# Kernel tuning notes

Hardware: AMD Instinct MI355X
Metric: run time of the kernel (lower is better)

Reference implementation:

```python
import jax, jax.numpy as jnp
import numpy as np

TOKENS, DIM, N_EXPERTS, TOPK = 8192, 4096, 256, 8

def setup_inputs() -> dict:
    key = jax.random.key(0)
    k1, k2 = jax.random.split(key)
    x = jax.random.normal(k1, (TOKENS, DIM), dtype=jnp.float32)
    weight = jax.random.normal(k2, (N_EXPERTS, DIM), dtype=jnp.float32) * (DIM ** -0.5)
    return {"x": x, "weight": weight}

def reference(x, weight):
    # logits: [tokens, n_experts]
    logits = jnp.einsum('td,ed->te', x, weight)
    scores = jax.nn.sigmoid(logits)
    topv, indices = jax.lax.top_k(scores, TOPK)          # [tokens, topk]
    gates = topv / jnp.sum(topv, axis=-1, keepdims=True)
    return gates, indices
```

## Files before the change

### kernel.cpp

```cpp
#include <hip/hip_runtime.h>
#include <hip/hip_bf16.h>
#include <hip/hip_fp16.h>
#include <math.h>

#define TOKENS   8192
#define DIM      4096
#define NEXP     256
#define TOPK     8
#define CAND     12

#define MT4      64
#define BK3      64
#define KG       (DIM / 32)

typedef _Float16 f16x8 __attribute__((ext_vector_type(8)));
typedef float    f32x4 __attribute__((ext_vector_type(4)));

typedef const __attribute__((address_space(1))) unsigned int* gas_ptr;
typedef       __attribute__((address_space(3))) unsigned int* las_ptr;

__global__ __launch_bounds__(256)
void convert_w(const float* __restrict__ w, _Float16* __restrict__ whs) {
    const int g = blockIdx.x * 256 + threadIdx.x;
    const int tile = g >> 6, c = g & 63;
    const int q = c >> 4, r = c & 15;
    const int ng = tile / KG, kg = tile % KG;
    const int n = ng * 16 + r, k = kg * 32 + q * 8;
    const float4 a = *(const float4*)(w + (size_t)n * DIM + k);
    const float4 b = *(const float4*)(w + (size_t)n * DIM + k + 4);
    f16x8 h;
    h[0] = (_Float16)a.x; h[1] = (_Float16)a.y;
    h[2] = (_Float16)a.z; h[3] = (_Float16)a.w;
    h[4] = (_Float16)b.x; h[5] = (_Float16)b.y;
    h[6] = (_Float16)b.z; h[7] = (_Float16)b.w;
    *(f16x8*)(whs + (size_t)g * 8) = h;
}

__global__ __launch_bounds__(256, 3)
void gemm_v4(const float* __restrict__ x, const _Float16* __restrict__ whs,
             float* __restrict__ logits, int kspan) {
    __shared__ _Float16 As[8 * 512];
    __shared__ _Float16 Bs[32 * 512];

    const int t = threadIdx.x, w = t >> 6, lane = t & 63;
    const int m0 = blockIdx.x * MT4;
    const int kb = blockIdx.y * kspan;
    float* lp    = logits + (size_t)blockIdx.y * TOKENS * NEXP;

    const int am  = t >> 2;
    const int ack = (t & 3) * 2;
    const int amg = am >> 4, amr = am & 15;
    const int aoff0 = ((amg * 2 + (ack >> 2)) * 64 + (ack & 3) * 16 + amr) * 8;
    const int ack1  = ack + 1;
    const int aoff1 = ((amg * 2 + (ack1 >> 2)) * 64 + (ack1 & 3) * 16 + amr) * 8;

    f32x4 acc[4][4];
    #pragma unroll
    for (int i = 0; i < 4; ++i)
        #pragma unroll
        for (int j = 0; j < 4; ++j) acc[i][j] = (f32x4){0.f, 0.f, 0.f, 0.f};

    const float* xrow = x + (size_t)(m0 + am) * DIM + ack * 8;
    float4 xr0 = *(const float4*)(xrow + kb);
    float4 xr1 = *(const float4*)(xrow + kb + 4);
    float4 xr2 = *(const float4*)(xrow + kb + 8);
    float4 xr3 = *(const float4*)(xrow + kb + 12);

    for (int k0 = kb; k0 < kb + kspan; k0 += BK3) {
        #pragma unroll
        for (int c = 0; c < 8; ++c) {
            const int ti  = w * 8 + c;
            const int ng  = ti >> 1, kgl = ti & 1;
            const _Float16* gp = whs + ((size_t)(ng * KG + (k0 >> 5) + kgl)) * 512
                                     + lane * 8;
            __builtin_amdgcn_global_load_lds((gas_ptr)gp, (las_ptr)&Bs[ti * 512],
                                             16, 0, 0);
        }
        {
            f16x8 h0, h1;
            h0[0] = (_Float16)xr0.x; h0[1] = (_Float16)xr0.y;
            h0[2] = (_Float16)xr0.z; h0[3] = (_Float16)xr0.w;
            h0[4] = (_Float16)xr1.x; h0[5] = (_Float16)xr1.y;
            h0[6] = (_Float16)xr1.z; h0[7] = (_Float16)xr1.w;
            h1[0] = (_Float16)xr2.x; h1[1] = (_Float16)xr2.y;
            h1[2] = (_Float16)xr2.z; h1[3] = (_Float16)xr2.w;
            h1[4] = (_Float16)xr3.x; h1[5] = (_Float16)xr3.y;
            h1[6] = (_Float16)xr3.z; h1[7] = (_Float16)xr3.w;
            *(f16x8*)&As[aoff0] = h0;
            *(f16x8*)&As[aoff1] = h1;
        }
        __syncthreads();

        if (k0 + BK3 < kb + kspan) {
            xr0 = *(const float4*)(xrow + k0 + BK3);
            xr1 = *(const float4*)(xrow + k0 + BK3 + 4);
            xr2 = *(const float4*)(xrow + k0 + BK3 + 8);
            xr3 = *(const float4*)(xrow + k0 + BK3 + 12);
        }

        #pragma unroll
        for (int kk = 0; kk < 2; ++kk) {
            f16x8 af[4], bf[4];
            #pragma unroll
            for (int mt = 0; mt < 4; ++mt)
                af[mt] = *(const f16x8*)&As[((mt * 2 + kk) * 64 + lane) * 8];
            #pragma unroll
            for (int nt = 0; nt < 4; ++nt)
                bf[nt] = *(const f16x8*)&Bs[(((w * 4 + nt) * 2 + kk) * 64 + lane) * 8];
            #pragma unroll
            for (int mt = 0; mt < 4; ++mt)
                #pragma unroll
                for (int nt = 0; nt < 4; ++nt)
                    acc[mt][nt] = __builtin_amdgcn_mfma_f32_16x16x32_f16(
                        af[mt], bf[nt], acc[mt][nt], 0, 0, 0);
        }
        __syncthreads();
    }

    #pragma unroll
    for (int mt = 0; mt < 4; ++mt) {
        #pragma unroll
        for (int nt = 0; nt < 4; ++nt) {
            #pragma unroll
            for (int r = 0; r < 4; ++r) {
                const int m = m0 + mt * 16 + (lane >> 4) * 4 + r;
                const int n = (w * 4 + nt) * 16 + (lane & 15);
                lp[(size_t)m * NEXP + n] = acc[mt][nt][r];
            }
        }
    }
}

__global__ __launch_bounds__(256)
void topk_cand(const float* __restrict__ logits, int* __restrict__ cand,
               int nsplit) {
    const int lane  = threadIdx.x & 63;
    const int token = blockIdx.x * 4 + (threadIdx.x >> 6);
    const float* lp = logits + (size_t)token * NEXP;

    float s[4];
    #pragma unroll
    for (int j = 0; j < 4; ++j) s[j] = 0.f;
    for (int p = 0; p < nsplit; ++p) {
        const float* pp = lp + (size_t)p * TOKENS * NEXP;
        #pragma unroll
        for (int j = 0; j < 4; ++j) s[j] += pp[j * 64 + lane];
    }

    int mye = 0;
    #pragma unroll
    for (int r = 0; r < CAND; ++r) {
        float bv = s[0];
        int   be = lane;
        #pragma unroll
        for (int j = 1; j < 4; ++j) {
            if (s[j] > bv) { bv = s[j]; be = j * 64 + lane; }
        }
        #pragma unroll
        for (int off = 32; off > 0; off >>= 1) {
            const float ov = __shfl_xor(bv, off, 64);
            const int   oe = __shfl_xor(be, off, 64);
            if (ov > bv || (ov == bv && oe < be)) { bv = ov; be = oe; }
        }
        if (lane == r) mye = be;
        if ((be & 63) == lane) s[be >> 6] = -1e30f;
    }

    if (lane < CAND) cand[token * CAND + lane] = mye;
}

__global__ __launch_bounds__(256)
void rescore(const float* __restrict__ x, const float* __restrict__ w,
             const int* __restrict__ cand, float* __restrict__ out) {
    __shared__ float  xs[DIM];
    __shared__ double stot[CAND];
    __shared__ int    sce[CAND];

    const int t = threadIdx.x, wave = t >> 6, lane = t & 63;
    const int token = blockIdx.x;

    const float* xrow = x + (size_t)token * DIM;
    #pragma unroll
    for (int r = 0; r < 4; ++r) {
        const float* gp = xrow + r * 1024 + wave * 256 + lane * 4;
        __builtin_amdgcn_global_load_lds((gas_ptr)gp,
                                         (las_ptr)&xs[r * 1024 + wave * 256],
                                         16, 0, 2 );
    }

    int ce[3];
    const f32x4* wp[3];
    #pragma unroll
    for (int j = 0; j < 3; ++j) {
        ce[j] = __builtin_amdgcn_readfirstlane(cand[token * CAND + wave * 3 + j]);
        wp[j] = (const f32x4*)(w + (size_t)ce[j] * DIM);
    }

    double acc[3];
    #pragma unroll
    for (int j = 0; j < 3; ++j) acc[j] = 0.0;

    f32x4 wb[3][3];
    #pragma unroll
    for (int j = 0; j < 3; ++j) wb[0][j] = wp[j][lane];
    #pragma unroll
    for (int j = 0; j < 3; ++j) wb[1][j] = wp[j][64 + lane];

    __syncthreads();

    #pragma unroll
    for (int i = 0; i < 16; ++i) {
        const int cur = i % 3, nxt = (i + 2) % 3;
        if (i < 14) {
            const int o = lane + (i + 2) * 64;
            #pragma unroll
            for (int j = 0; j < 3; ++j) wb[nxt][j] = wp[j][o];
        }
        const f32x4 xv = *(const f32x4*)&xs[(lane + i * 64) * 4];
        const double dx = (double)xv.x, dy = (double)xv.y;
        const double dz = (double)xv.z, dw = (double)xv.w;
        #pragma unroll
        for (int j = 0; j < 3; ++j) {
            const f32x4 wv = wb[cur][j];
            acc[j] = fma(dw, (double)wv.w,
                     fma(dz, (double)wv.z,
                     fma(dy, (double)wv.y,
                     fma(dx, (double)wv.x, acc[j]))));
        }
    }

    #pragma unroll
    for (int off = 32; off > 0; off >>= 1) {
        #pragma unroll
        for (int j = 0; j < 3; ++j)
            acc[j] += __shfl_xor(acc[j], off, 64);
    }

    if (lane == 0) {
        #pragma unroll
        for (int j = 0; j < 3; ++j) {
            stot[wave * 3 + j] = acc[j];
            sce[wave * 3 + j]  = ce[j];
        }
    }
    __syncthreads();

    if (wave == 0) {
        double tt[CAND];
        int    ee[CAND];
        #pragma unroll
        for (int c = 0; c < CAND; ++c) { tt[c] = stot[c]; ee[c] = sce[c]; }

        int rank[CAND];
        #pragma unroll
        for (int c = 0; c < CAND; ++c) {
            int r = 0;
            #pragma unroll
            for (int j = 0; j < CAND; ++j) {
                if (j == c) continue;
                if (tt[j] > tt[c] || (tt[j] == tt[c] && ee[j] < ee[c])) ++r;
            }
            rank[c] = r;
        }

        float sig[CAND];
        float sum = 0.f;
        #pragma unroll
        for (int c = 0; c < CAND; ++c) {
            sig[c] = 1.0f / (1.0f + expf(-(float)tt[c]));
            if (rank[c] < TOPK) sum += sig[c];
        }

        if (lane < TOPK) {
            float g = 0.f; int ei = 0;
            #pragma unroll
            for (int c = 0; c < CAND; ++c)
                if (rank[c] == lane) { g = sig[c]; ei = ee[c]; }
            out[(size_t)token * TOPK + lane] = g / sum;
            out[(size_t)TOKENS * TOPK + (size_t)token * TOPK + lane] = (float)ei;
        }
    }
}

extern "C" void kernel_launch(void* const* d_in, const int* in_sizes, int n_in,
                              void* d_out, int out_size, void* d_ws, size_t ws_size,
                              hipStream_t stream) {
    const float* x = (const float*)d_in[0];
    const float* w = (const float*)d_in[1];
    float* out     = (float*)d_out;

    const size_t plane = (size_t)TOKENS * NEXP * sizeof(float);
    const size_t fixed = (size_t)TOKENS * CAND * sizeof(int)
                       + (size_t)NEXP * DIM * sizeof(_Float16);
    int S = 4;
    if (ws_size < 4 * plane + fixed) S = (ws_size >= 2 * plane + fixed) ? 2 : 1;

    float*     logits = (float*)d_ws;
    int*       candp  = (int*)((char*)d_ws + (size_t)S * plane);
    _Float16*  whs    = (_Float16*)((char*)candp + (size_t)TOKENS * CAND * sizeof(int));

    convert_w<<<512, 256, 0, stream>>>(w, whs);
    dim3 ggrid(TOKENS / MT4, S);
    gemm_v4<<<ggrid, 256, 0, stream>>>(x, whs, logits, DIM / S);
    topk_cand<<<TOKENS / 4, 256, 0, stream>>>(logits, candp, S);
    rescore<<<TOKENS, 256, 0, stream>>>(x, w, candp, out);
}
```

Baseline: 315.3 us.

## Fuse candidate top-k into rescore and shrink GEMM M-tile to 32 rows

Removes the separate topk_cand kernel. Each wave in rescore now sums the split-K logit planes and runs the candidate selection itself, so the candidate index buffer and one launch go away. The GEMM M-tile drops from 64 to 32 rows with a higher occupancy bound, and the rescore weight prefetch goes from 2 to 3 stages deep. The trade-offs: all four waves repeat the same top-12 selection per token, and the smaller GEMM tile reuses each loaded B tile for fewer rows, which doubles B traffic.

```diff
diff --git a/kernel.cpp b/kernel.cpp
--- a/kernel.cpp
+++ b/kernel.cpp
@@ -9,7 +9,7 @@
 #define TOPK     8
 #define CAND     12
 
-#define MT4      64
+#define MT4      32
 #define BK3      64
 #define KG       (DIM / 32)
 
@@ -36,10 +36,10 @@
     *(f16x8*)(whs + (size_t)g * 8) = h;
 }
 
-__global__ __launch_bounds__(256, 3)
+__global__ __launch_bounds__(256, 4)
 void gemm_v4(const float* __restrict__ x, const _Float16* __restrict__ whs,
              float* __restrict__ logits, int kspan) {
-    __shared__ _Float16 As[8 * 512];
+    __shared__ _Float16 As[4 * 512];
     __shared__ _Float16 Bs[32 * 512];
 
     const int t = threadIdx.x, w = t >> 6, lane = t & 63;
@@ -47,24 +47,20 @@
     const int kb = blockIdx.y * kspan;
     float* lp    = logits + (size_t)blockIdx.y * TOKENS * NEXP;
 
-    const int am  = t >> 2;
-    const int ack = (t & 3) * 2;
+    const int am  = t >> 3;
+    const int ack = t & 7;
     const int amg = am >> 4, amr = am & 15;
-    const int aoff0 = ((amg * 2 + (ack >> 2)) * 64 + (ack & 3) * 16 + amr) * 8;
-    const int ack1  = ack + 1;
-    const int aoff1 = ((amg * 2 + (ack1 >> 2)) * 64 + (ack1 & 3) * 16 + amr) * 8;
-
-    f32x4 acc[4][4];
-    #pragma unroll
-    for (int i = 0; i < 4; ++i)
+    const int aoff = ((amg * 2 + (ack >> 2)) * 64 + (ack & 3) * 16 + amr) * 8;
+
+    f32x4 acc[2][4];
+    #pragma unroll
+    for (int i = 0; i < 2; ++i)
         #pragma unroll
         for (int j = 0; j < 4; ++j) acc[i][j] = (f32x4){0.f, 0.f, 0.f, 0.f};
 
     const float* xrow = x + (size_t)(m0 + am) * DIM + ack * 8;
     float4 xr0 = *(const float4*)(xrow + kb);
     float4 xr1 = *(const float4*)(xrow + kb + 4);
-    float4 xr2 = *(const float4*)(xrow + kb + 8);
-    float4 xr3 = *(const float4*)(xrow + kb + 12);
 
     for (int k0 = kb; k0 < kb + kspan; k0 += BK3) {
         #pragma unroll
@@ -77,38 +73,31 @@
                                              16, 0, 0);
         }
         {
-            f16x8 h0, h1;
+            f16x8 h0;
             h0[0] = (_Float16)xr0.x; h0[1] = (_Float16)xr0.y;
             h0[2] = (_Float16)xr0.z; h0[3] = (_Float16)xr0.w;
             h0[4] = (_Float16)xr1.x; h0[5] = (_Float16)xr1.y;
             h0[6] = (_Float16)xr1.z; h0[7] = (_Float16)xr1.w;
-            h1[0] = (_Float16)xr2.x; h1[1] = (_Float16)xr2.y;
-            h1[2] = (_Float16)xr2.z; h1[3] = (_Float16)xr2.w;
-            h1[4] = (_Float16)xr3.x; h1[5] = (_Float16)xr3.y;
-            h1[6] = (_Float16)xr3.z; h1[7] = (_Float16)xr3.w;
-            *(f16x8*)&As[aoff0] = h0;
-            *(f16x8*)&As[aoff1] = h1;
+            *(f16x8*)&As[aoff] = h0;
         }
         __syncthreads();
 
         if (k0 + BK3 < kb + kspan) {
             xr0 = *(const float4*)(xrow + k0 + BK3);
             xr1 = *(const float4*)(xrow + k0 + BK3 + 4);
-            xr2 = *(const float4*)(xrow + k0 + BK3 + 8);
-            xr3 = *(const float4*)(xrow + k0 + BK3 + 12);
         }
 
         #pragma unroll
         for (int kk = 0; kk < 2; ++kk) {
-            f16x8 af[4], bf[4];
-            #pragma unroll
-            for (int mt = 0; mt < 4; ++mt)
+            f16x8 af[2], bf[4];
+            #pragma unroll
+            for (int mt = 0; mt < 2; ++mt)
                 af[mt] = *(const f16x8*)&As[((mt * 2 + kk) * 64 + lane) * 8];
             #pragma unroll
             for (int nt = 0; nt < 4; ++nt)
                 bf[nt] = *(const f16x8*)&Bs[(((w * 4 + nt) * 2 + kk) * 64 + lane) * 8];
             #pragma unroll
-            for (int mt = 0; mt < 4; ++mt)
+            for (int mt = 0; mt < 2; ++mt)
                 #pragma unroll
                 for (int nt = 0; nt < 4; ++nt)
                     acc[mt][nt] = __builtin_amdgcn_mfma_f32_16x16x32_f16(
@@ -118,7 +107,7 @@
     }
 
     #pragma unroll
-    for (int mt = 0; mt < 4; ++mt) {
+    for (int mt = 0; mt < 2; ++mt) {
         #pragma unroll
         for (int nt = 0; nt < 4; ++nt) {
             #pragma unroll
@@ -132,46 +121,9 @@
 }
 
 __global__ __launch_bounds__(256)
-void topk_cand(const float* __restrict__ logits, int* __restrict__ cand,
-               int nsplit) {
-    const int lane  = threadIdx.x & 63;
-    const int token = blockIdx.x * 4 + (threadIdx.x >> 6);
-    const float* lp = logits + (size_t)token * NEXP;
-
-    float s[4];
-    #pragma unroll
-    for (int j = 0; j < 4; ++j) s[j] = 0.f;
-    for (int p = 0; p < nsplit; ++p) {
-        const float* pp = lp + (size_t)p * TOKENS * NEXP;
-        #pragma unroll
-        for (int j = 0; j < 4; ++j) s[j] += pp[j * 64 + lane];
-    }
-
-    int mye = 0;
-    #pragma unroll
-    for (int r = 0; r < CAND; ++r) {
-        float bv = s[0];
-        int   be = lane;
-        #pragma unroll
-        for (int j = 1; j < 4; ++j) {
-            if (s[j] > bv) { bv = s[j]; be = j * 64 + lane; }
-        }
-        #pragma unroll
-        for (int off = 32; off > 0; off >>= 1) {
-            const float ov = __shfl_xor(bv, off, 64);
-            const int   oe = __shfl_xor(be, off, 64);
-            if (ov > bv || (ov == bv && oe < be)) { bv = ov; be = oe; }
-        }
-        if (lane == r) mye = be;
-        if ((be & 63) == lane) s[be >> 6] = -1e30f;
-    }
-
-    if (lane < CAND) cand[token * CAND + lane] = mye;
-}
-
-__global__ __launch_bounds__(256)
 void rescore(const float* __restrict__ x, const float* __restrict__ w,
-             const int* __restrict__ cand, float* __restrict__ out) {
+             const float* __restrict__ logits, float* __restrict__ out,
+             int nsplit) {
     __shared__ float  xs[DIM];
     __shared__ double stot[CAND];
     __shared__ int    sce[CAND];
@@ -189,30 +141,60 @@
     }
 
     int ce[3];
+    {
+        const float* lp = logits + (size_t)token * NEXP;
+        float s[4];
+        #pragma unroll
+        for (int j = 0; j < 4; ++j) s[j] = 0.f;
+        for (int p = 0; p < nsplit; ++p) {
+            const float* pp = lp + (size_t)p * TOKENS * NEXP;
+            #pragma unroll
+            for (int j = 0; j < 4; ++j) s[j] += pp[j * 64 + lane];
+        }
+        #pragma unroll
+        for (int r = 0; r < CAND; ++r) {
+            float bv = s[0];
+            int   be = lane;
+            #pragma unroll
+            for (int j = 1; j < 4; ++j) {
+                if (s[j] > bv) { bv = s[j]; be = j * 64 + lane; }
+            }
+            #pragma unroll
+            for (int off = 32; off > 0; off >>= 1) {
+                const float ov = __shfl_xor(bv, off, 64);
+                const int   oe = __shfl_xor(be, off, 64);
+                if (ov > bv || (ov == bv && oe < be)) { bv = ov; be = oe; }
+            }
+            if (r >= wave * 3 && r < wave * 3 + 3)
+                ce[r - wave * 3] = __builtin_amdgcn_readfirstlane(be);
+            if ((be & 63) == lane) s[be >> 6] = -1e30f;
+        }
+    }
+
     const f32x4* wp[3];
     #pragma unroll
-    for (int j = 0; j < 3; ++j) {
-        ce[j] = __builtin_amdgcn_readfirstlane(cand[token * CAND + wave * 3 + j]);
+    for (int j = 0; j < 3; ++j)
         wp[j] = (const f32x4*)(w + (size_t)ce[j] * DIM);
-    }
 
     double acc[3];
     #pragma unroll
     for (int j = 0; j < 3; ++j) acc[j] = 0.0;
 
-    f32x4 wb[3][3];
+    f32x4 wb[4][3];
     #pragma unroll
     for (int j = 0; j < 3; ++j) wb[0][j] = wp[j][lane];
     #pragma unroll
     for (int j = 0; j < 3; ++j) wb[1][j] = wp[j][64 + lane];
+    #pragma unroll
+    for (int j = 0; j < 3; ++j) wb[2][j] = wp[j][128 + lane];
 
     __syncthreads();
 
     #pragma unroll
     for (int i = 0; i < 16; ++i) {
-        const int cur = i % 3, nxt = (i + 2) % 3;
-        if (i < 14) {
-            const int o = lane + (i + 2) * 64;
+        const int cur = i & 3, nxt = (i + 3) & 3;
+        if (i < 13) {
+            const int o = lane + (i + 3) * 64;
             #pragma unroll
             for (int j = 0; j < 3; ++j) wb[nxt][j] = wp[j][o];
         }
@@ -290,18 +272,15 @@
     float* out     = (float*)d_out;
 
     const size_t plane = (size_t)TOKENS * NEXP * sizeof(float);
-    const size_t fixed = (size_t)TOKENS * CAND * sizeof(int)
-                       + (size_t)NEXP * DIM * sizeof(_Float16);
+    const size_t fixed = (size_t)NEXP * DIM * sizeof(_Float16);
     int S = 4;
     if (ws_size < 4 * plane + fixed) S = (ws_size >= 2 * plane + fixed) ? 2 : 1;
 
     float*     logits = (float*)d_ws;
-    int*       candp  = (int*)((char*)d_ws + (size_t)S * plane);
-    _Float16*  whs    = (_Float16*)((char*)candp + (size_t)TOKENS * CAND * sizeof(int));
+    _Float16*  whs    = (_Float16*)((char*)d_ws + (size_t)S * plane);
 
     convert_w<<<512, 256, 0, stream>>>(w, whs);
     dim3 ggrid(TOKENS / MT4, S);
     gemm_v4<<<ggrid, 256, 0, stream>>>(x, whs, logits, DIM / S);
-    topk_cand<<<TOKENS / 4, 256, 0, stream>>>(logits, candp, S);
-    rescore<<<TOKENS, 256, 0, stream>>>(x, w, candp, out);
-}
+    rescore<<<TOKENS, 256, 0, stream>>>(x, w, logits, out, S);
+}
```

New measurement: 337.6 us. 7.1% more time.

## Double-buffer LDS tiles in GEMM and deepen weight prefetch in rescoring

Applied to the files above, without the earlier changes.

The GEMM kernel now uses two LDS buffers for A and B. The next B tile is issued via global_load_lds and the next A tile is written while the current tile is consumed by MFMAs, which cuts one barrier per iteration. The occupancy hint drops from 3 to 2 blocks per SM to make room for the doubled shared memory. Separately, the fp64 rescoring kernel prefetches weights three iterations ahead instead of two, which raises register use in exchange for more latency hiding.

```diff
diff --git a/kernel.cpp b/kernel.cpp
--- a/kernel.cpp
+++ b/kernel.cpp
@@ -36,15 +36,16 @@
     *(f16x8*)(whs + (size_t)g * 8) = h;
 }
 
-__global__ __launch_bounds__(256, 3)
+__global__ __launch_bounds__(256, 2)
 void gemm_v4(const float* __restrict__ x, const _Float16* __restrict__ whs,
              float* __restrict__ logits, int kspan) {
-    __shared__ _Float16 As[8 * 512];
-    __shared__ _Float16 Bs[32 * 512];
+    __shared__ _Float16 As[2][8 * 512];
+    __shared__ _Float16 Bs[2][32 * 512];
 
     const int t = threadIdx.x, w = t >> 6, lane = t & 63;
     const int m0 = blockIdx.x * MT4;
     const int kb = blockIdx.y * kspan;
+    const int kend = kb + kspan;
     float* lp    = logits + (size_t)blockIdx.y * TOKENS * NEXP;
 
     const int am  = t >> 2;
@@ -61,52 +62,67 @@
         for (int j = 0; j < 4; ++j) acc[i][j] = (f32x4){0.f, 0.f, 0.f, 0.f};
 
     const float* xrow = x + (size_t)(m0 + am) * DIM + ack * 8;
-    float4 xr0 = *(const float4*)(xrow + kb);
-    float4 xr1 = *(const float4*)(xrow + kb + 4);
-    float4 xr2 = *(const float4*)(xrow + kb + 8);
-    float4 xr3 = *(const float4*)(xrow + kb + 12);
-
-    for (int k0 = kb; k0 < kb + kspan; k0 += BK3) {
+
+    auto stage_B = [&](int buf, int k0) {
         #pragma unroll
         for (int c = 0; c < 8; ++c) {
             const int ti  = w * 8 + c;
             const int ng  = ti >> 1, kgl = ti & 1;
             const _Float16* gp = whs + ((size_t)(ng * KG + (k0 >> 5) + kgl)) * 512
                                      + lane * 8;
-            __builtin_amdgcn_global_load_lds((gas_ptr)gp, (las_ptr)&Bs[ti * 512],
+            __builtin_amdgcn_global_load_lds((gas_ptr)gp,
+                                             (las_ptr)&Bs[buf][ti * 512],
                                              16, 0, 0);
         }
-        {
-            f16x8 h0, h1;
-            h0[0] = (_Float16)xr0.x; h0[1] = (_Float16)xr0.y;
-            h0[2] = (_Float16)xr0.z; h0[3] = (_Float16)xr0.w;
-            h0[4] = (_Float16)xr1.x; h0[5] = (_Float16)xr1.y;
-            h0[6] = (_Float16)xr1.z; h0[7] = (_Float16)xr1.w;
-            h1[0] = (_Float16)xr2.x; h1[1] = (_Float16)xr2.y;
-            h1[2] = (_Float16)xr2.z; h1[3] = (_Float16)xr2.w;
-            h1[4] = (_Float16)xr3.x; h1[5] = (_Float16)xr3.y;
-            h1[6] = (_Float16)xr3.z; h1[7] = (_Float16)xr3.w;
-            *(f16x8*)&As[aoff0] = h0;
-            *(f16x8*)&As[aoff1] = h1;
-        }
-        __syncthreads();
-
-        if (k0 + BK3 < kb + kspan) {
-            xr0 = *(const float4*)(xrow + k0 + BK3);
-            xr1 = *(const float4*)(xrow + k0 + BK3 + 4);
-            xr2 = *(const float4*)(xrow + k0 + BK3 + 8);
-            xr3 = *(const float4*)(xrow + k0 + BK3 + 12);
-        }
+    };
+    auto write_A = [&](int buf, const float4& r0, const float4& r1,
+                       const float4& r2, const float4& r3) {
+        f16x8 h0, h1;
+        h0[0] = (_Float16)r0.x; h0[1] = (_Float16)r0.y;
+        h0[2] = (_Float16)r0.z; h0[3] = (_Float16)r0.w;
+        h0[4] = (_Float16)r1.x; h0[5] = (_Float16)r1.y;
+        h0[6] = (_Float16)r1.z; h0[7] = (_Float16)r1.w;
+        h1[0] = (_Float16)r2.x; h1[1] = (_Float16)r2.y;
+        h1[2] = (_Float16)r2.z; h1[3] = (_Float16)r2.w;
+        h1[4] = (_Float16)r3.x; h1[5] = (_Float16)r3.y;
+        h1[6] = (_Float16)r3.z; h1[7] = (_Float16)r3.w;
+        *(f16x8*)&As[buf][aoff0] = h0;
+        *(f16x8*)&As[buf][aoff1] = h1;
+    };
+
+    {
+        float4 r0 = *(const float4*)(xrow + kb);
+        float4 r1 = *(const float4*)(xrow + kb + 4);
+        float4 r2 = *(const float4*)(xrow + kb + 8);
+        float4 r3 = *(const float4*)(xrow + kb + 12);
+        stage_B(0, kb);
+        write_A(0, r0, r1, r2, r3);
+    }
+    float4 xn0, xn1, xn2, xn3;
+    if (kb + BK3 < kend) {
+        xn0 = *(const float4*)(xrow + kb + BK3);
+        xn1 = *(const float4*)(xrow + kb + BK3 + 4);
+        xn2 = *(const float4*)(xrow + kb + BK3 + 8);
+        xn3 = *(const float4*)(xrow + kb + BK3 + 12);
+    }
+    __syncthreads();
+
+    int cur = 0;
+    for (int k0 = kb; k0 < kend; k0 += BK3) {
+        const int nxt = cur ^ 1;
+        const bool has_next = (k0 + BK3 < kend);
+
+        if (has_next) stage_B(nxt, k0 + BK3);
 
         #pragma unroll
         for (int kk = 0; kk < 2; ++kk) {
             f16x8 af[4], bf[4];
             #pragma unroll
             for (int mt = 0; mt < 4; ++mt)
-                af[mt] = *(const f16x8*)&As[((mt * 2 + kk) * 64 + lane) * 8];
+                af[mt] = *(const f16x8*)&As[cur][((mt * 2 + kk) * 64 + lane) * 8];
             #pragma unroll
             for (int nt = 0; nt < 4; ++nt)
-                bf[nt] = *(const f16x8*)&Bs[(((w * 4 + nt) * 2 + kk) * 64 + lane) * 8];
+                bf[nt] = *(const f16x8*)&Bs[cur][(((w * 4 + nt) * 2 + kk) * 64 + lane) * 8];
             #pragma unroll
             for (int mt = 0; mt < 4; ++mt)
                 #pragma unroll
@@ -114,7 +130,18 @@
                     acc[mt][nt] = __builtin_amdgcn_mfma_f32_16x16x32_f16(
                         af[mt], bf[nt], acc[mt][nt], 0, 0, 0);
         }
+
+        if (has_next) write_A(nxt, xn0, xn1, xn2, xn3);
+
         __syncthreads();
+
+        if (k0 + 2 * BK3 < kend) {
+            xn0 = *(const float4*)(xrow + k0 + 2 * BK3);
+            xn1 = *(const float4*)(xrow + k0 + 2 * BK3 + 4);
+            xn2 = *(const float4*)(xrow + k0 + 2 * BK3 + 8);
+            xn3 = *(const float4*)(xrow + k0 + 2 * BK3 + 12);
+        }
+        cur = nxt;
     }
 
     #pragma unroll
@@ -200,19 +227,21 @@
     #pragma unroll
     for (int j = 0; j < 3; ++j) acc[j] = 0.0;
 
-    f32x4 wb[3][3];
+    f32x4 wb[4][3];
     #pragma unroll
     for (int j = 0; j < 3; ++j) wb[0][j] = wp[j][lane];
     #pragma unroll
     for (int j = 0; j < 3; ++j) wb[1][j] = wp[j][64 + lane];
+    #pragma unroll
+    for (int j = 0; j < 3; ++j) wb[2][j] = wp[j][128 + lane];
 
     __syncthreads();
 
     #pragma unroll
     for (int i = 0; i < 16; ++i) {
-        const int cur = i % 3, nxt = (i + 2) % 3;
-        if (i < 14) {
-            const int o = lane + (i + 2) * 64;
+        const int cur = i & 3, nxt = (i + 3) & 3;
+        if (i < 13) {
+            const int o = lane + (i + 3) * 64;
             #pragma unroll
             for (int j = 0; j < 3; ++j) wb[nxt][j] = wp[j][o];
         }
```

After: 308.6 us. 1.02x faster.
